# Performance work log

Hardware: AMD Instinct MI355X
Metric: run time of the kernel (lower is better)

## Reference

```python
import jax, jax.numpy as jnp
import numpy as np

N_NODES = 20000
N_EDGES = 40000
N_GRAPHS = 500
D_IN = 32     # initial_dim_gcn
D_E = 16      # edge_dim_feature
H1 = 100      # hidden_dim_nn_1
H2 = 20       # hidden_dim_nn_2
F1 = 50       # hidden_dim_fcn_1


def setup_inputs() -> dict:
    key = jax.random.key(0)
    ks = jax.random.split(key, 16)
    s = lambda k, shp, fan: (jax.random.normal(k, shp, jnp.float32) / np.sqrt(fan)).astype(jnp.float32)
    return {
        "x": jax.random.normal(ks[0], (N_NODES, D_IN), jnp.float32),
        "edge_attr": jax.random.normal(ks[1], (N_EDGES, D_E), jnp.float32),
        "edge_index": jax.random.randint(ks[2], (2, N_EDGES), 0, N_NODES, jnp.int64),
        "batch": jnp.sort(jax.random.randint(ks[3], (N_NODES,), 0, N_GRAPHS, jnp.int64)),
        # NNConv layer 1: edge MLP Linear(D_E -> D_IN*H1), root weight, bias
        "nn1_W": s(ks[4], (D_E, D_IN * H1), D_E),
        "nn1_b": jnp.zeros((D_IN * H1,), jnp.float32),
        "root1": s(ks[5], (D_IN, H1), D_IN),
        "bias1": jnp.zeros((H1,), jnp.float32),
        # NNConv layer 2: edge MLP Linear(D_E -> H1*H2), root weight, bias
        "nn2_W": s(ks[6], (D_E, H1 * H2), D_E),
        "nn2_b": jnp.zeros((H1 * H2,), jnp.float32),
        "root2": s(ks[7], (H1, H2), H1),
        "bias2": jnp.zeros((H2,), jnp.float32),
        # FCN head
        "lin1_W": s(ks[8], (H2, F1), H2),
        "lin1_b": jnp.zeros((F1,), jnp.float32),
        "lin2_W": s(ks[9], (F1, 1), F1),
        "lin2_b": jnp.zeros((1,), jnp.float32),
    }


def _nnconv(x, src, dst, edge_attr, nnW, nnb, root, bias, d_in, d_out):
    # per-edge weight matrices: [E, d_in, d_out]
    theta = (edge_attr @ nnW + nnb).reshape(-1, d_in, d_out)
    # gather source features, per-edge matmul, scatter-add to targets
    msg = jnp.einsum('ei,eio->eo', x[src], theta)            # [E, d_out]
    agg = jax.ops.segment_sum(msg, dst, num_segments=x.shape[0])
    return agg + x @ root + bias


def reference(x, edge_attr, edge_index, batch,
              nn1_W, nn1_b, root1, bias1,
              nn2_W, nn2_b, root2, bias2,
              lin1_W, lin1_b, lin2_W, lin2_b):
    src, dst = edge_index[0], edge_index[1]  # PyG: message from j=src, aggregate at i=dst
    h = jax.nn.relu(_nnconv(x, src, dst, edge_attr, nn1_W, nn1_b, root1, bias1, D_IN, H1))
    h = jax.nn.relu(_nnconv(h, src, dst, edge_attr, nn2_W, nn2_b, root2, bias2, H1, H2))
    g = jax.ops.segment_sum(h, batch, num_segments=N_GRAPHS)  # sum-pool readout [G, H2]
    g = jax.nn.relu(g @ lin1_W + lin1_b)
    out = g @ lin2_W + lin2_b
    return out.reshape(-1)
```

## Files before the change

### kernel.cpp

```cpp
#include <hip/hip_runtime.h>
#include <hip/hip_bf16.h>
#include <hip/hip_fp16.h>

#define N_NODES 20000
#define N_EDGES 40000
#define N_GRAPHS 500
#define D_IN 32
#define D_E 16
#define H1 100
#define H2 20
#define F1 50

#define EB1 64
#define YNB 12
#define ET3 12

using h2f = __attribute__((ext_vector_type(2))) _Float16;
using h8f = __attribute__((ext_vector_type(8))) _Float16;
using f4  = __attribute__((ext_vector_type(4))) float;

__global__ __launch_bounds__(256) void prep_kernel(
    const float* __restrict__ nn1W, const float* __restrict__ nn1b,
    const float* __restrict__ nn2W, const float* __restrict__ nn2b,
    unsigned short* __restrict__ Wfrag, float* __restrict__ Bext,
    float* __restrict__ zbase)
{
  const int tid = blockIdx.x * 256 + threadIdx.x;
  if (tid < 544 * 112) {
    const int c  = tid / 3584;
    const int r  = tid % 3584;
    const int to = r / 512;
    const int l  = (r % 512) >> 3;
    const int j  = r & 7;
    const int i  = (l >> 4) * 8 + j;
    const int o  = to * 16 + (l & 15);
    float v = 0.f;
    if (o < H1) v = (c < 16) ? nn1W[c * (D_IN * H1) + i * H1 + o] : nn1b[i * H1 + o];
    _Float16 hv = (_Float16)v;
    Wfrag[tid] = __builtin_bit_cast(unsigned short, hv);
  } else if (tid < 544 * 112 + H1 * 340) {
    const int idx = tid - 544 * 112;
    const int i = idx / 340, j = idx % 340;
    const int k = j / H2, o = j % H2;
    Bext[idx] = (k < 16) ? nn2W[k * (H1 * H2) + i * H2 + o] : nn2b[i * H2 + o];
  }
  float4* zp = (float4*)zbase;
  for (int i = tid; i < 602500; i += 512 * 256)
    zp[i] = make_float4(0.f, 0.f, 0.f, 0.f);
}

__global__ __launch_bounds__(256, 2) void edge1_kernel(
    const float* __restrict__ x, const float* __restrict__ ea,
    const int* __restrict__ eidx, const unsigned short* __restrict__ Wfrag,
    float* __restrict__ agg1)
{
  __shared__ uint4 Plds[4 * 64];
  __shared__ uint4 Blds[2][7 * 64];
  __shared__ int   sdst[EB1];

  const int t    = threadIdx.x;
  const int lane = t & 63;
  const int w    = t >> 6;
  const int e0   = blockIdx.x * EB1;

  const int e_loc = t >> 2;
  const int jg    = t & 3;
  const int src   = eidx[e0 + e_loc];

  h2f xh[4];
  {
    const float4* xp = (const float4*)&x[(size_t)src * D_IN + jg * 8];
    float4 v0 = xp[0], v1 = xp[1];
    float xf[8] = {v0.x, v0.y, v0.z, v0.w, v1.x, v1.y, v1.z, v1.w};
    #pragma unroll
    for (int j = 0; j < 4; ++j) {
      h2f p; p[0] = (_Float16)xf[2*j]; p[1] = (_Float16)xf[2*j+1]; xh[j] = p;
    }
  }
  _Float16 eh[17];
  {
    const float4* ep = (const float4*)&ea[(size_t)(e0 + e_loc) * D_E];
    float4 v0 = ep[0], v1 = ep[1], v2 = ep[2], v3 = ep[3];
    float ef[16] = {v0.x,v0.y,v0.z,v0.w, v1.x,v1.y,v1.z,v1.w,
                    v2.x,v2.y,v2.z,v2.w, v3.x,v3.y,v3.z,v3.w};
    #pragma unroll
    for (int k = 0; k < 16; ++k) eh[k] = (_Float16)ef[k];
    eh[16] = (_Float16)1.0f;
  }
  if (t < EB1) sdst[t] = eidx[N_EDGES + e0 + t];

  const uint4* __restrict__ Bf = (const uint4*)Wfrag;

  {
    uint4 s0 = Bf[t];
    uint4 s1;
    if (t < 192) s1 = Bf[256 + t];
    Blds[0][t] = s0;
    if (t < 192) Blds[0][256 + t] = s1;
  }
  __syncthreads();

  f4 acc[7];
  #pragma unroll
  for (int to = 0; to < 7; ++to) acc[to] = f4{0.f, 0.f, 0.f, 0.f};

  const int pslot = w * 64 + (e_loc & 15) + 16 * jg;

  #pragma unroll
  for (int c = 0; c < 17; ++c) {
    uint4 s0, s1;
    if (c < 16) {
      const uint4* bn = Bf + (c + 1) * 448;
      s0 = bn[t];
      if (t < 192) s1 = bn[256 + t];
    }

    h2f es; es[0] = eh[c]; es[1] = eh[c];
    unsigned int pk[4];
    #pragma unroll
    for (int j = 0; j < 4; ++j) {
      h2f pr = xh[j] * es;
      pk[j] = __builtin_bit_cast(unsigned int, pr);
    }
    Plds[pslot] = make_uint4(pk[0], pk[1], pk[2], pk[3]);

    uint4 a = Plds[w * 64 + lane];
    h8f A = __builtin_bit_cast(h8f, a);

    const uint4* bb = &Blds[c & 1][0];
    #pragma unroll
    for (int to = 0; to < 7; ++to) {
      h8f B = __builtin_bit_cast(h8f, bb[to * 64 + lane]);
      acc[to] = __builtin_amdgcn_mfma_f32_16x16x32_f16(A, B, acc[to], 0, 0, 0);
    }

    if (c < 16) {
      Blds[(c + 1) & 1][t] = s0;
      if (t < 192) Blds[(c + 1) & 1][256 + t] = s1;
    }
    __syncthreads();
  }

  const int col = lane & 15, rowg = lane >> 4;
  #pragma unroll
  for (int r = 0; r < 4; ++r) {
    const int el = w * 16 + rowg * 4 + r;
    const int d = sdst[el];
    float* ap = agg1 + (size_t)d * H1;
    #pragma unroll
    for (int to = 0; to < 7; ++to) {
      const int o = to * 16 + col;
      if (o < H1) atomicAdd(&ap[o], acc[to][r]);
    }
  }
}

__global__ __launch_bounds__(256) void y2h1_kernel(
    const float* __restrict__ x, const float* __restrict__ agg1,
    const float* __restrict__ root1, const float* __restrict__ bias1,
    const float* __restrict__ Bext, float* __restrict__ h1,
    float* __restrict__ Y2)
{
  __shared__ float sroot1[D_IN * H1];
  __shared__ float sxl[YNB * D_IN];
  __shared__ __align__(16) float hT[H1][YNB];
  const int t  = threadIdx.x;
  const int n0 = blockIdx.x * YNB;

  for (int idx = t; idx < 800; idx += 256)
    *(float4*)&sroot1[idx * 4] = *(const float4*)&root1[idx * 4];
  if (t < 96) {
    const int fo = t * 4;
    const int nn = fo >> 5;
    float4 v = make_float4(0.f, 0.f, 0.f, 0.f);
    if (n0 + nn < N_NODES) v = *(const float4*)&x[(size_t)n0 * D_IN + fo];
    *(float4*)&sxl[fo] = v;
  }
  __syncthreads();

  for (int idx = t; idx < YNB * H1; idx += 256) {
    const int nn = idx / H1, i = idx - nn * H1;
    const int n = n0 + nn;
    float v = 0.f;
    if (n < N_NODES) {
      v = agg1[(size_t)n0 * H1 + idx] + bias1[i];
      #pragma unroll 8
      for (int d = 0; d < D_IN; ++d)
        v = fmaf(sxl[nn * D_IN + d], sroot1[d * H1 + i], v);
      v = fmaxf(v, 0.f);
      h1[(size_t)n0 * H1 + idx] = v;
    }
    hT[i][nn] = v;
  }
  __syncthreads();

  const int jg = t % 85;
  const int ng = t / 85;
  if (ng < 3) {
    const int j0 = jg * 4;
    const float* __restrict__ bp = Bext + j0;
    float acc[4][4];
    #pragma unroll
    for (int r = 0; r < 4; ++r)
      #pragma unroll
      for (int cc = 0; cc < 4; ++cc) acc[r][cc] = 0.f;

    #pragma unroll 2
    for (int i = 0; i < H1; ++i) {
      const float4 bv = *(const float4*)&bp[i * 340];
      const float4 hv = *(const float4*)&hT[i][ng * 4];
      acc[0][0] = fmaf(hv.x, bv.x, acc[0][0]);
      acc[0][1] = fmaf(hv.x, bv.y, acc[0][1]);
      acc[0][2] = fmaf(hv.x, bv.z, acc[0][2]);
      acc[0][3] = fmaf(hv.x, bv.w, acc[0][3]);
      acc[1][0] = fmaf(hv.y, bv.x, acc[1][0]);
      acc[1][1] = fmaf(hv.y, bv.y, acc[1][1]);
      acc[1][2] = fmaf(hv.y, bv.z, acc[1][2]);
      acc[1][3] = fmaf(hv.y, bv.w, acc[1][3]);
      acc[2][0] = fmaf(hv.z, bv.x, acc[2][0]);
      acc[2][1] = fmaf(hv.z, bv.y, acc[2][1]);
      acc[2][2] = fmaf(hv.z, bv.z, acc[2][2]);
      acc[2][3] = fmaf(hv.z, bv.w, acc[2][3]);
      acc[3][0] = fmaf(hv.w, bv.x, acc[3][0]);
      acc[3][1] = fmaf(hv.w, bv.y, acc[3][1]);
      acc[3][2] = fmaf(hv.w, bv.z, acc[3][2]);
      acc[3][3] = fmaf(hv.w, bv.w, acc[3][3]);
    }
    const int nb = n0 + ng * 4;
    #pragma unroll
    for (int r = 0; r < 4; ++r) {
      const int n = nb + r;
      if (n < N_NODES)
        *(float4*)&Y2[(size_t)n * 340 + j0] =
            make_float4(acc[r][0], acc[r][1], acc[r][2], acc[r][3]);
    }
  }
}

__global__ __launch_bounds__(256) void edge2_kernel(
    const float* __restrict__ ea, const int* __restrict__ eidx,
    const float* __restrict__ Y2, float* __restrict__ agg2)
{
  __shared__ __align__(16) float sy[ET3][344];
  __shared__ float se[ET3][16];
  __shared__ int sd[ET3];
  const int t  = threadIdx.x;
  const int e0 = blockIdx.x * ET3;

  if (t < ET3) {
    const int e = e0 + t;
    sd[t] = (e < N_EDGES) ? eidx[N_EDGES + e] : -1;
  }
  for (int idx = t; idx < ET3 * 4; idx += 256) {
    const int el = idx >> 2, q = idx & 3;
    const int e = e0 + el;
    if (e < N_EDGES)
      *(float4*)&se[el][q * 4] = *(const float4*)&ea[(size_t)e * D_E + q * 4];
  }
  for (int idx = t; idx < ET3 * 85; idx += 256) {
    const int el = idx / 85, q = idx - el * 85;
    const int e = e0 + el;
    if (e < N_EDGES) {
      const int s = eidx[e];
      *(float4*)&sy[el][q * 4] = *(const float4*)&Y2[(size_t)s * 340 + q * 4];
    }
  }
  __syncthreads();

  const int el = t / H2, o = t % H2;
  const int e = e0 + el;
  if (el < ET3 && e < N_EDGES) {
    float m = sy[el][320 + o];
    #pragma unroll
    for (int k = 0; k < D_E; ++k)
      m = fmaf(se[el][k], sy[el][k * 20 + o], m);
    atomicAdd(&agg2[(size_t)sd[el] * H2 + o], m);
  }
}

__global__ __launch_bounds__(256) void node2_pool_kernel(
    const float* __restrict__ h1, const float* __restrict__ agg2,
    const float* __restrict__ root2, const float* __restrict__ bias2,
    const int* __restrict__ batch, float* __restrict__ g)
{
  __shared__ float sroot[H1 * H2];
  __shared__ float sv[ET3][H2];
  __shared__ int   sg[ET3];
  const int t  = threadIdx.x;
  const int n0 = blockIdx.x * ET3;

  for (int idx = t; idx < (H1 * H2) / 4; idx += 256)
    *(float4*)&sroot[idx * 4] = *(const float4*)&root2[idx * 4];
  if (t < ET3) {
    const int n = n0 + t;
    sg[t] = (n < N_NODES) ? batch[n] : -1;
  }
  __syncthreads();

  const int nl = t / H2, o = t % H2;
  const int n = n0 + nl;
  if (nl < ET3) {
    float v = 0.f;
    if (n < N_NODES) {
      v = agg2[(size_t)n * H2 + o] + bias2[o];
      const float* hr = &h1[(size_t)n * H1];
      #pragma unroll 5
      for (int i = 0; i < H1; i += 4) {
        const float4 hv = *(const float4*)&hr[i];
        v = fmaf(hv.x, sroot[(i    ) * H2 + o], v);
        v = fmaf(hv.y, sroot[(i + 1) * H2 + o], v);
        v = fmaf(hv.z, sroot[(i + 2) * H2 + o], v);
        v = fmaf(hv.w, sroot[(i + 3) * H2 + o], v);
      }
      v = fmaxf(v, 0.f);
    }
    sv[nl][o] = v;
  }
  __syncthreads();

  if (t < H2) {
    float run = 0.f;
    int cur = sg[0];
    #pragma unroll
    for (int r = 0; r < ET3; ++r) {
      const int gid = sg[r];
      if (gid != cur) {
        if (cur >= 0) atomicAdd(&g[cur * H2 + t], run);
        run = 0.f; cur = gid;
      }
      run += sv[r][t];
    }
    if (cur >= 0) atomicAdd(&g[cur * H2 + t], run);
  }
}

__global__ __launch_bounds__(64) void final_kernel(
    const float* __restrict__ g, const float* __restrict__ lin1W,
    const float* __restrict__ lin1b, const float* __restrict__ lin2W,
    const float* __restrict__ lin2b, float* __restrict__ out)
{
  const int gr = blockIdx.x;
  const int tt = threadIdx.x;
  float v = 0.f;
  if (tt < F1) {
    float s = lin1b[tt];
    #pragma unroll
    for (int o = 0; o < H2; ++o) s = fmaf(g[gr * H2 + o], lin1W[o * F1 + tt], s);
    v = fmaxf(s, 0.f) * lin2W[tt];
  }
  #pragma unroll
  for (int off = 32; off > 0; off >>= 1) v += __shfl_down(v, off, 64);
  if (tt == 0) out[gr] = v + lin2b[0];
}

extern "C" void kernel_launch(void* const* d_in, const int* in_sizes, int n_in,
                              void* d_out, int out_size, void* d_ws, size_t ws_size,
                              hipStream_t stream) {
  const float* x     = (const float*)d_in[0];
  const float* ea    = (const float*)d_in[1];
  const int*   eidx  = (const int*)d_in[2];
  const int*   batch = (const int*)d_in[3];
  const float* nn1W  = (const float*)d_in[4];
  const float* nn1b  = (const float*)d_in[5];
  const float* root1 = (const float*)d_in[6];
  const float* bias1 = (const float*)d_in[7];
  const float* nn2W  = (const float*)d_in[8];
  const float* nn2b  = (const float*)d_in[9];
  const float* root2 = (const float*)d_in[10];
  const float* bias2 = (const float*)d_in[11];
  const float* lin1W = (const float*)d_in[12];
  const float* lin1b = (const float*)d_in[13];
  const float* lin2W = (const float*)d_in[14];
  const float* lin2b = (const float*)d_in[15];
  float* out = (float*)d_out;

  float* ws   = (float*)d_ws;
  float* agg1 = ws;
  float* agg2 = agg1 + N_NODES * H1;
  float* g    = agg2 + N_NODES * H2;
  float* h1   = g    + N_GRAPHS * H2;
  float* spare= h1   + N_NODES * H1;
  float* Y2   = spare+ N_NODES * H2;
  float* Bext = spare;
  unsigned short* Wfrag = (unsigned short*)(Y2 + (size_t)N_NODES * 340 - 30464);

  prep_kernel<<<512, 256, 0, stream>>>(nn1W, nn1b, nn2W, nn2b, Wfrag, Bext, agg1);
  edge1_kernel<<<N_EDGES / EB1, 256, 0, stream>>>(x, ea, eidx, Wfrag, agg1);
  y2h1_kernel<<<(N_NODES + YNB - 1) / YNB, 256, 0, stream>>>(
      x, agg1, root1, bias1, Bext, h1, Y2);
  edge2_kernel<<<(N_EDGES + ET3 - 1) / ET3, 256, 0, stream>>>(ea, eidx, Y2, agg2);
  node2_pool_kernel<<<(N_NODES + ET3 - 1) / ET3, 256, 0, stream>>>(
      h1, agg2, root2, bias2, batch, g);
  final_kernel<<<N_GRAPHS, 64, 0, stream>>>(g, lin1W, lin1b, lin2W, lin2b, out);
}
```

Baseline: 182.7 us.

## Replace node-side Y2 precompute with per-edge fp16 MFMA for layer-2 NNConv

Removes the per-node Y2 = h1·Bext precomputation (a 20000x340 fp32 intermediate) and the gather-based edge2 kernel. Layer-2 messages are now computed per edge with fp16 MFMA, the same way layer 1 already is. Each thread scales its gathered h1 row by an edge attribute, and the kernel contracts that against prepacked fp16 nn2 weight fragments double-buffered in LDS. This avoids writing and re-reading the large Y2 buffer, but adds fp16 rounding on h1 and on the layer-2 weights, plus more per-edge arithmetic.

```diff
diff --git a/kernel.cpp b/kernel.cpp
--- a/kernel.cpp
+++ b/kernel.cpp
@@ -22,7 +22,7 @@
 __global__ __launch_bounds__(256) void prep_kernel(
     const float* __restrict__ nn1W, const float* __restrict__ nn1b,
     const float* __restrict__ nn2W, const float* __restrict__ nn2b,
-    unsigned short* __restrict__ Wfrag, float* __restrict__ Bext,
+    unsigned short* __restrict__ Wfrag1, unsigned short* __restrict__ Wfrag2,
     float* __restrict__ zbase)
 {
   const int tid = blockIdx.x * 256 + threadIdx.x;
@@ -37,12 +37,21 @@
     float v = 0.f;
     if (o < H1) v = (c < 16) ? nn1W[c * (D_IN * H1) + i * H1 + o] : nn1b[i * H1 + o];
     _Float16 hv = (_Float16)v;
-    Wfrag[tid] = __builtin_bit_cast(unsigned short, hv);
-  } else if (tid < 544 * 112 + H1 * 340) {
-    const int idx = tid - 544 * 112;
-    const int i = idx / 340, j = idx % 340;
-    const int k = j / H2, o = j % H2;
-    Bext[idx] = (k < 16) ? nn2W[k * (H1 * H2) + i * H2 + o] : nn2b[i * H2 + o];
+    Wfrag1[tid] = __builtin_bit_cast(unsigned short, hv);
+  } else if (tid < 544 * 112 + 17 * 4096) {
+    const int t2 = tid - 544 * 112;
+    const int c  = t2 >> 12;
+    const int q  = (t2 >> 10) & 3;
+    const int to = (t2 >> 9) & 1;
+    const int l  = (t2 >> 3) & 63;
+    const int j  = t2 & 7;
+    const int i  = q * 32 + (l >> 4) * 8 + j;
+    const int o  = to * 16 + (l & 15);
+    float v = 0.f;
+    if (i < H1 && o < H2)
+      v = (c < 16) ? nn2W[c * (H1 * H2) + i * H2 + o] : nn2b[i * H2 + o];
+    _Float16 hv = (_Float16)v;
+    Wfrag2[t2] = __builtin_bit_cast(unsigned short, hv);
   }
   float4* zp = (float4*)zbase;
   for (int i = tid; i < 602500; i += 512 * 256)
@@ -155,15 +164,13 @@
   }
 }
 
-__global__ __launch_bounds__(256) void y2h1_kernel(
+__global__ __launch_bounds__(256) void node1_kernel(
     const float* __restrict__ x, const float* __restrict__ agg1,
     const float* __restrict__ root1, const float* __restrict__ bias1,
-    const float* __restrict__ Bext, float* __restrict__ h1,
-    float* __restrict__ Y2)
+    float* __restrict__ h1)
 {
   __shared__ float sroot1[D_IN * H1];
   __shared__ float sxl[YNB * D_IN];
-  __shared__ __align__(16) float hT[H1][YNB];
   const int t  = threadIdx.x;
   const int n0 = blockIdx.x * YNB;
 
@@ -181,100 +188,140 @@
   for (int idx = t; idx < YNB * H1; idx += 256) {
     const int nn = idx / H1, i = idx - nn * H1;
     const int n = n0 + nn;
-    float v = 0.f;
     if (n < N_NODES) {
-      v = agg1[(size_t)n0 * H1 + idx] + bias1[i];
+      float v = agg1[(size_t)n0 * H1 + idx] + bias1[i];
       #pragma unroll 8
       for (int d = 0; d < D_IN; ++d)
         v = fmaf(sxl[nn * D_IN + d], sroot1[d * H1 + i], v);
-      v = fmaxf(v, 0.f);
-      h1[(size_t)n0 * H1 + idx] = v;
-    }
-    hT[i][nn] = v;
+      h1[(size_t)n0 * H1 + idx] = fmaxf(v, 0.f);
+    }
+  }
+}
+
+__global__ __launch_bounds__(256, 2) void edge2m_kernel(
+    const float* __restrict__ h1, const float* __restrict__ ea,
+    const int* __restrict__ eidx, const unsigned short* __restrict__ Wfrag2,
+    float* __restrict__ agg2)
+{
+  __shared__ uint4 Plds[4][4][64];
+  __shared__ uint4 Blds[2][512];
+  __shared__ int   sdst[EB1];
+
+  const int t    = threadIdx.x;
+  const int lane = t & 63;
+  const int w    = t >> 6;
+  const int e0   = blockIdx.x * EB1;
+
+  const int e_loc = t >> 2;
+  const int jg    = t & 3;
+  const int m     = e_loc & 15;
+  const int src   = eidx[e0 + e_loc];
+
+  h2f xh[16];
+  {
+    float xf[32];
+    const float* hp = &h1[(size_t)src * H1 + jg * 32];
+    if (jg < 3) {
+      #pragma unroll
+      for (int q4 = 0; q4 < 8; ++q4) {
+        float4 v = *(const float4*)&hp[q4 * 4];
+        xf[q4*4+0] = v.x; xf[q4*4+1] = v.y; xf[q4*4+2] = v.z; xf[q4*4+3] = v.w;
+      }
+    } else {
+      float4 v = *(const float4*)hp;
+      xf[0] = v.x; xf[1] = v.y; xf[2] = v.z; xf[3] = v.w;
+      #pragma unroll
+      for (int ii = 4; ii < 32; ++ii) xf[ii] = 0.f;
+    }
+    #pragma unroll
+    for (int j2 = 0; j2 < 16; ++j2) {
+      h2f p; p[0] = (_Float16)xf[2*j2]; p[1] = (_Float16)xf[2*j2+1]; xh[j2] = p;
+    }
+  }
+  _Float16 eh[17];
+  {
+    const float4* ep = (const float4*)&ea[(size_t)(e0 + e_loc) * D_E];
+    float4 v0 = ep[0], v1 = ep[1], v2 = ep[2], v3 = ep[3];
+    float ef[16] = {v0.x,v0.y,v0.z,v0.w, v1.x,v1.y,v1.z,v1.w,
+                    v2.x,v2.y,v2.z,v2.w, v3.x,v3.y,v3.z,v3.w};
+    #pragma unroll
+    for (int k = 0; k < 16; ++k) eh[k] = (_Float16)ef[k];
+    eh[16] = (_Float16)1.0f;
+  }
+  if (t < EB1) sdst[t] = eidx[N_EDGES + e0 + t];
+
+  const uint4* __restrict__ Bf = (const uint4*)Wfrag2;
+
+  {
+    uint4 s0 = Bf[t];
+    uint4 s1 = Bf[256 + t];
+    Blds[0][t] = s0;
+    Blds[0][256 + t] = s1;
+  }
+  {
+    h2f es; es[0] = eh[0]; es[1] = eh[0];
+    unsigned int pk[16];
+    #pragma unroll
+    for (int j2 = 0; j2 < 16; ++j2) {
+      h2f pr = xh[j2] * es;
+      pk[j2] = __builtin_bit_cast(unsigned int, pr);
+    }
+    #pragma unroll
+    for (int oc = 0; oc < 4; ++oc)
+      Plds[w][jg][16 * oc + m] = make_uint4(pk[4*oc], pk[4*oc+1], pk[4*oc+2], pk[4*oc+3]);
   }
   __syncthreads();
 
-  const int jg = t % 85;
-  const int ng = t / 85;
-  if (ng < 3) {
-    const int j0 = jg * 4;
-    const float* __restrict__ bp = Bext + j0;
-    float acc[4][4];
-    #pragma unroll
-    for (int r = 0; r < 4; ++r)
+  f4 acc0 = f4{0.f, 0.f, 0.f, 0.f};
+  f4 acc1 = f4{0.f, 0.f, 0.f, 0.f};
+
+  #pragma unroll
+  for (int c = 0; c < 17; ++c) {
+    const int buf = c & 1;
+    uint4 s0, s1;
+    if (c < 16) {
+      const uint4* bn = Bf + (c + 1) * 512;
+      s0 = bn[t];
+      s1 = bn[256 + t];
+    }
+
+    #pragma unroll
+    for (int q = 0; q < 4; ++q) {
+      uint4 a  = Plds[w][q][lane];
+      uint4 b0 = Blds[buf][q * 128 + lane];
+      uint4 b1 = Blds[buf][q * 128 + 64 + lane];
+      h8f A  = __builtin_bit_cast(h8f, a);
+      h8f B0 = __builtin_bit_cast(h8f, b0);
+      h8f B1 = __builtin_bit_cast(h8f, b1);
+      acc0 = __builtin_amdgcn_mfma_f32_16x16x32_f16(A, B0, acc0, 0, 0, 0);
+      acc1 = __builtin_amdgcn_mfma_f32_16x16x32_f16(A, B1, acc1, 0, 0, 0);
+    }
+
+    if (c < 16) {
+      h2f es; es[0] = eh[c + 1]; es[1] = eh[c + 1];
+      unsigned int pk[16];
       #pragma unroll
-      for (int cc = 0; cc < 4; ++cc) acc[r][cc] = 0.f;
-
-    #pragma unroll 2
-    for (int i = 0; i < H1; ++i) {
-      const float4 bv = *(const float4*)&bp[i * 340];
-      const float4 hv = *(const float4*)&hT[i][ng * 4];
-      acc[0][0] = fmaf(hv.x, bv.x, acc[0][0]);
-      acc[0][1] = fmaf(hv.x, bv.y, acc[0][1]);
-      acc[0][2] = fmaf(hv.x, bv.z, acc[0][2]);
-      acc[0][3] = fmaf(hv.x, bv.w, acc[0][3]);
-      acc[1][0] = fmaf(hv.y, bv.x, acc[1][0]);
-      acc[1][1] = fmaf(hv.y, bv.y, acc[1][1]);
-      acc[1][2] = fmaf(hv.y, bv.z, acc[1][2]);
-      acc[1][3] = fmaf(hv.y, bv.w, acc[1][3]);
-      acc[2][0] = fmaf(hv.z, bv.x, acc[2][0]);
-      acc[2][1] = fmaf(hv.z, bv.y, acc[2][1]);
-      acc[2][2] = fmaf(hv.z, bv.z, acc[2][2]);
-      acc[2][3] = fmaf(hv.z, bv.w, acc[2][3]);
-      acc[3][0] = fmaf(hv.w, bv.x, acc[3][0]);
-      acc[3][1] = fmaf(hv.w, bv.y, acc[3][1]);
-      acc[3][2] = fmaf(hv.w, bv.z, acc[3][2]);
-      acc[3][3] = fmaf(hv.w, bv.w, acc[3][3]);
-    }
-    const int nb = n0 + ng * 4;
-    #pragma unroll
-    for (int r = 0; r < 4; ++r) {
-      const int n = nb + r;
-      if (n < N_NODES)
-        *(float4*)&Y2[(size_t)n * 340 + j0] =
-            make_float4(acc[r][0], acc[r][1], acc[r][2], acc[r][3]);
-    }
-  }
-}
-
-__global__ __launch_bounds__(256) void edge2_kernel(
-    const float* __restrict__ ea, const int* __restrict__ eidx,
-    const float* __restrict__ Y2, float* __restrict__ agg2)
-{
-  __shared__ __align__(16) float sy[ET3][344];
-  __shared__ float se[ET3][16];
-  __shared__ int sd[ET3];
-  const int t  = threadIdx.x;
-  const int e0 = blockIdx.x * ET3;
-
-  if (t < ET3) {
-    const int e = e0 + t;
-    sd[t] = (e < N_EDGES) ? eidx[N_EDGES + e] : -1;
-  }
-  for (int idx = t; idx < ET3 * 4; idx += 256) {
-    const int el = idx >> 2, q = idx & 3;
-    const int e = e0 + el;
-    if (e < N_EDGES)
-      *(float4*)&se[el][q * 4] = *(const float4*)&ea[(size_t)e * D_E + q * 4];
-  }
-  for (int idx = t; idx < ET3 * 85; idx += 256) {
-    const int el = idx / 85, q = idx - el * 85;
-    const int e = e0 + el;
-    if (e < N_EDGES) {
-      const int s = eidx[e];
-      *(float4*)&sy[el][q * 4] = *(const float4*)&Y2[(size_t)s * 340 + q * 4];
-    }
-  }
-  __syncthreads();
-
-  const int el = t / H2, o = t % H2;
-  const int e = e0 + el;
-  if (el < ET3 && e < N_EDGES) {
-    float m = sy[el][320 + o];
-    #pragma unroll
-    for (int k = 0; k < D_E; ++k)
-      m = fmaf(se[el][k], sy[el][k * 20 + o], m);
-    atomicAdd(&agg2[(size_t)sd[el] * H2 + o], m);
+      for (int j2 = 0; j2 < 16; ++j2) {
+        h2f pr = xh[j2] * es;
+        pk[j2] = __builtin_bit_cast(unsigned int, pr);
+      }
+      #pragma unroll
+      for (int oc = 0; oc < 4; ++oc)
+        Plds[w][jg][16 * oc + m] = make_uint4(pk[4*oc], pk[4*oc+1], pk[4*oc+2], pk[4*oc+3]);
+      Blds[buf ^ 1][t] = s0;
+      Blds[buf ^ 1][256 + t] = s1;
+      __syncthreads();
+    }
+  }
+
+  const int col = lane & 15, rowg = lane >> 4;
+  #pragma unroll
+  for (int r = 0; r < 4; ++r) {
+    const int el = w * 16 + rowg * 4 + r;
+    const int d  = sdst[el];
+    float* ap = agg2 + (size_t)d * H2;
+    atomicAdd(&ap[col], acc0[r]);
+    if (col < 4) atomicAdd(&ap[16 + col], acc1[r]);
   }
 }
 
@@ -379,16 +426,14 @@
   float* agg2 = agg1 + N_NODES * H1;
   float* g    = agg2 + N_NODES * H2;
   float* h1   = g    + N_GRAPHS * H2;
-  float* spare= h1   + N_NODES * H1;
-  float* Y2   = spare+ N_NODES * H2;
-  float* Bext = spare;
-  unsigned short* Wfrag = (unsigned short*)(Y2 + (size_t)N_NODES * 340 - 30464);
-
-  prep_kernel<<<512, 256, 0, stream>>>(nn1W, nn1b, nn2W, nn2b, Wfrag, Bext, agg1);
-  edge1_kernel<<<N_EDGES / EB1, 256, 0, stream>>>(x, ea, eidx, Wfrag, agg1);
-  y2h1_kernel<<<(N_NODES + YNB - 1) / YNB, 256, 0, stream>>>(
-      x, agg1, root1, bias1, Bext, h1, Y2);
-  edge2_kernel<<<(N_EDGES + ET3 - 1) / ET3, 256, 0, stream>>>(ea, eidx, Y2, agg2);
+  unsigned short* Wfrag1 = (unsigned short*)(h1 + (size_t)N_NODES * H1);
+  unsigned short* Wfrag2 = Wfrag1 + 61440;
+
+  prep_kernel<<<512, 256, 0, stream>>>(nn1W, nn1b, nn2W, nn2b, Wfrag1, Wfrag2, agg1);
+  edge1_kernel<<<N_EDGES / EB1, 256, 0, stream>>>(x, ea, eidx, Wfrag1, agg1);
+  node1_kernel<<<(N_NODES + YNB - 1) / YNB, 256, 0, stream>>>(
+      x, agg1, root1, bias1, h1);
+  edge2m_kernel<<<N_EDGES / EB1, 256, 0, stream>>>(h1, ea, eidx, Wfrag2, agg2);
   node2_pool_kernel<<<(N_NODES + ET3 - 1) / ET3, 256, 0, stream>>>(
       h1, agg2, root2, bias2, batch, g);
   final_kernel<<<N_GRAPHS, 64, 0, stream>>>(g, lin1W, lin1b, lin2W, lin2b, out);
```

After: 172.8 us. -5.5%, faster.
